# Kernel optimization log

Measured on AMD Instinct MI355X. Metric: run time of the kernel, lower is better.

Reference implementation:

```python
import jax, jax.numpy as jnp
import numpy as np

N_NODES = 100000
N_EDGES = 1600000
D_IN, D_HID, D_OUT = 128, 128, 128
EPS = 1e-12  # torch F.normalize eps


def _sage_conv(x, src, dst, Wl, bl, Wr):
    # PyG SAGEConv, aggr='mean', normalize=True:
    #   out = lin_l(mean_{j in N(i)} x_j) + lin_r(x_i); out = l2_normalize(out)
    msg = x[src]                                             # [E, D] gather
    agg = jax.ops.segment_sum(msg, dst, num_segments=N_NODES)
    cnt = jax.ops.segment_sum(jnp.ones((msg.shape[0],), x.dtype), dst,
                              num_segments=N_NODES)
    agg = agg / jnp.maximum(cnt, 1.0)[:, None]               # scatter-mean
    out = agg @ Wl + bl + x @ Wr
    norm = jnp.linalg.norm(out, axis=-1, keepdims=True)
    return out / jnp.maximum(norm, EPS)


def setup_inputs() -> dict:
    key = jax.random.key(0)
    ks = jax.random.split(key, 8)
    x = jax.random.normal(ks[0], (N_NODES, D_IN), dtype=jnp.float32)
    edge_index = jax.random.randint(ks[1], (2, N_EDGES), 0, N_NODES, dtype=jnp.int64)
    s1 = 1.0 / np.sqrt(D_IN)
    s2 = 1.0 / np.sqrt(D_HID)
    return {
        "x": x,
        "edge_index": edge_index,
        "W1l": jax.random.uniform(ks[2], (D_IN, D_HID), jnp.float32, -s1, s1),
        "b1": jnp.zeros((D_HID,), jnp.float32),
        "W1r": jax.random.uniform(ks[3], (D_IN, D_HID), jnp.float32, -s1, s1),
        "W2l": jax.random.uniform(ks[4], (D_HID, D_OUT), jnp.float32, -s2, s2),
        "b2": jnp.zeros((D_OUT,), jnp.float32),
        "W2r": jax.random.uniform(ks[5], (D_HID, D_OUT), jnp.float32, -s2, s2),
    }


def reference(x, edge_index, W1l, b1, W1r, W2l, b2, W2r):
    src, dst = edge_index[0], edge_index[1]
    h = _sage_conv(x, src, dst, W1l, b1, W1r)
    h = jax.nn.relu(h)
    # dropout is identity at inference (F.dropout with training=False)
    out = _sage_conv(h, src, dst, W2l, b2, W2r)
    return out
```

## Files before the change

### kernel.cpp

```cpp
#include <hip/hip_runtime.h>

static constexpr int D = 128;
static constexpr int CHUNK = 2048;
static constexpr int EB = 4096;
static constexpr int BSH = 8;

typedef __attribute__((ext_vector_type(8))) short short8;
typedef __attribute__((ext_vector_type(4))) float f32x4;

__device__ inline ushort f2bf(float f) {
  union { float f; uint u; } x; x.f = f;
  uint r = (x.u + 0x7fffu + ((x.u >> 16) & 1u)) >> 16;
  return (ushort)r;
}
__device__ inline float bfhi(uint u) {
  union { uint u; float f; } x; x.u = u & 0xffff0000u;
  return x.f;
}
__device__ inline float bflo(uint u) {
  union { uint u; float f; } x; x.u = u << 16;
  return x.f;
}


__global__ __launch_bounds__(256) void bucket_hist_kernel(
    const int* __restrict__ dsts, int E, int NB, int* __restrict__ bhist) {
  __shared__ int h[512];
  for (int i = threadIdx.x; i < NB; i += 256) h[i] = 0;
  __syncthreads();
  int base = blockIdx.x * EB;
  for (int t = threadIdx.x; t < EB; t += 256) {
    int e = base + t;
    if (e < E) atomicAdd(&h[dsts[e] >> BSH], 1);
  }
  __syncthreads();
  for (int i = threadIdx.x; i < NB; i += 256)
    if (h[i]) atomicAdd(&bhist[i], h[i]);
}

__global__ __launch_bounds__(512) void bucket_scan_kernel(
    const int* __restrict__ bhist, int NB, int* __restrict__ bstart,
    int* __restrict__ bcursor) {
  __shared__ int arr[512];
  int t = threadIdx.x;
  int v = (t < NB) ? bhist[t] : 0;
  arr[t] = v;
  __syncthreads();
  for (int off = 1; off < 512; off <<= 1) {
    int u = (t >= off) ? arr[t - off] : 0;
    __syncthreads();
    arr[t] += u;
    __syncthreads();
  }
  if (t < NB) {
    int s = arr[t] - v;
    bstart[t] = s;
    bcursor[t] = s;
  }
  if (t == NB - 1) bstart[NB] = arr[t];
}

__global__ __launch_bounds__(256) void bin_scatter_kernel(
    const int* __restrict__ srcs, const int* __restrict__ dsts, int E, int NB,
    int* __restrict__ bcursor, uint* __restrict__ bucket_arr) {
  __shared__ int h[512];
  __shared__ int gpos[512];
  __shared__ int run[512];
  for (int i = threadIdx.x; i < NB; i += 256) { h[i] = 0; run[i] = 0; }
  __syncthreads();
  int base = blockIdx.x * EB;
  for (int t = threadIdx.x; t < EB; t += 256) {
    int e = base + t;
    if (e < E) atomicAdd(&h[dsts[e] >> BSH], 1);
  }
  __syncthreads();
  for (int i = threadIdx.x; i < NB; i += 256)
    gpos[i] = h[i] ? atomicAdd(&bcursor[i], h[i]) : 0;
  __syncthreads();
  for (int t = threadIdx.x; t < EB; t += 256) {
    int e = base + t;
    if (e < E) {
      int dst = dsts[e];
      int src = srcs[e];
      int b = dst >> BSH;
      int r = atomicAdd(&run[b], 1);
      bucket_arr[gpos[b] + r] = (uint)src | ((uint)(dst & 255) << 17);
    }
  }
}

__global__ __launch_bounds__(256) void bucket_deg_kernel(
    const uint* __restrict__ bucket_arr, const int* __restrict__ bstart,
    int* __restrict__ deg, int N) {
  __shared__ int dcnt[256];
  int b = blockIdx.x;
  int n0 = b << BSH;
  int nn = min(256, N - n0);
  if (threadIdx.x < nn) dcnt[threadIdx.x] = 0;
  __syncthreads();
  int s = bstart[b], e = bstart[b + 1];
  for (int t = s + threadIdx.x; t < e; t += 256)
    atomicAdd(&dcnt[bucket_arr[t] >> 17], 1);
  __syncthreads();
  if (threadIdx.x < nn) deg[n0 + threadIdx.x] = dcnt[threadIdx.x];
}

__global__ __launch_bounds__(256) void csr_scatter_kernel(
    const uint* __restrict__ bucket_arr, const int* __restrict__ bstart,
    const int* __restrict__ row_start, int* __restrict__ csr_src, int N) {
  __shared__ int cur[256];
  int b = blockIdx.x;
  int n0 = b << BSH;
  int nn = min(256, N - n0);
  if (threadIdx.x < nn) cur[threadIdx.x] = row_start[n0 + threadIdx.x];
  __syncthreads();
  int s = bstart[b], e = bstart[b + 1];
  for (int t = s + threadIdx.x; t < e; t += 256) {
    uint p = bucket_arr[t];
    int pos = atomicAdd(&cur[p >> 17], 1);
    csr_src[pos] = (int)(p & 0x1FFFFu);
  }
}


__global__ __launch_bounds__(256) void scan_partial(const int* __restrict__ deg,
                                                    int* __restrict__ bsum, int N) {
  int base = blockIdx.x * CHUNK;
  int s = 0;
  for (int i = threadIdx.x; i < CHUNK; i += 256) {
    int g = base + i;
    if (g < N) s += deg[g];
  }
  __shared__ int red[256];
  red[threadIdx.x] = s;
  __syncthreads();
  for (int off = 128; off; off >>= 1) {
    if (threadIdx.x < off) red[threadIdx.x] += red[threadIdx.x + off];
    __syncthreads();
  }
  if (threadIdx.x == 0) bsum[blockIdx.x] = red[0];
}

__global__ __launch_bounds__(256) void scan_bsum(int* __restrict__ bsum, int G,
                                                 int* __restrict__ row_end) {
  __shared__ int arr[256];
  int t = threadIdx.x;
  int v = (t < G) ? bsum[t] : 0;
  arr[t] = v;
  __syncthreads();
  for (int off = 1; off < 256; off <<= 1) {
    int u = (t >= off) ? arr[t - off] : 0;
    __syncthreads();
    arr[t] += u;
    __syncthreads();
  }
  if (t < G) bsum[t] = arr[t] - v;
  if (t == 255) *row_end = arr[255];
}

__global__ __launch_bounds__(256) void scan_final(const int* __restrict__ deg,
                                                  const int* __restrict__ bsum,
                                                  int* __restrict__ row_start, int N) {
  int tid = threadIdx.x;
  int base = blockIdx.x * CHUNK + tid * 8;
  int d[8];
  int ts = 0;
#pragma unroll
  for (int j = 0; j < 8; ++j) {
    int g = base + j;
    int t = (g < N) ? deg[g] : 0;
    d[j] = ts;
    ts += t;
  }
  __shared__ int arr[256];
  arr[tid] = ts;
  __syncthreads();
  for (int off = 1; off < 256; off <<= 1) {
    int u = (tid >= off) ? arr[tid - off] : 0;
    __syncthreads();
    arr[tid] += u;
    __syncthreads();
  }
  int off0 = bsum[blockIdx.x] + arr[tid] - ts;
#pragma unroll
  for (int j = 0; j < 8; ++j) {
    int g = base + j;
    if (g < N) row_start[g] = off0 + d[j];
  }
}


__global__ __launch_bounds__(256) void cvt_bf16(const float* __restrict__ in,
                                                ushort* __restrict__ outb, int n8) {
  int i = blockIdx.x * blockDim.x + threadIdx.x;
  if (i >= n8) return;
  float4 a = *reinterpret_cast<const float4*>(in + (size_t)i * 8);
  float4 b = *reinterpret_cast<const float4*>(in + (size_t)i * 8 + 4);
  union { ushort s[8]; short8 v; } o;
  o.s[0] = f2bf(a.x); o.s[1] = f2bf(a.y); o.s[2] = f2bf(a.z); o.s[3] = f2bf(a.w);
  o.s[4] = f2bf(b.x); o.s[5] = f2bf(b.y); o.s[6] = f2bf(b.z); o.s[7] = f2bf(b.w);
  *reinterpret_cast<short8*>(outb + (size_t)i * 8) = o.v;
}

__global__ __launch_bounds__(256) void wprep(const float* __restrict__ W,
                                             ushort* __restrict__ WT) {
  int e = blockIdx.x * 256 + threadIdx.x;
  int k = e >> 7, n = e & 127;
  WT[n * 128 + k] = f2bf(W[e]);
}


#define ACC8(P, M)                                   \
  acc[0] += (M) * bflo(P.x); acc[1] += (M) * bfhi(P.x); \
  acc[2] += (M) * bflo(P.y); acc[3] += (M) * bfhi(P.y); \
  acc[4] += (M) * bflo(P.z); acc[5] += (M) * bfhi(P.z); \
  acc[6] += (M) * bflo(P.w); acc[7] += (M) * bfhi(P.w);

__global__ __launch_bounds__(256) void agg_kernel_bf16(
    const ushort* __restrict__ xb, const int* __restrict__ row_start,
    const int* __restrict__ csr_src, ushort* __restrict__ aggb, int N) {
  int wid = (blockIdx.x * blockDim.x + threadIdx.x) >> 6;
  int lane = threadIdx.x & 63;
  if (wid >= N) return;
  int r0 = row_start[wid];
  int r1 = row_start[wid + 1];
  const int grp = lane >> 4;
  const int sub = lane & 15;
  float acc[8];
#pragma unroll
  for (int k = 0; k < 8; ++k) acc[k] = 0.f;

  for (int base = r0; base < r1; base += 64) {
    int cnt = min(64, r1 - base);
    int idx = (lane < cnt) ? csr_src[base + lane] : 0;
    for (int j = 0; j < cnt; j += 16) {
      int s0 = __shfl(idx, j + grp);
      int s1 = __shfl(idx, j + 4 + grp);
      int s2 = __shfl(idx, j + 8 + grp);
      int s3 = __shfl(idx, j + 12 + grp);
      float m0 = (j + grp < cnt) ? 1.f : 0.f;
      float m1 = (j + 4 + grp < cnt) ? 1.f : 0.f;
      float m2 = (j + 8 + grp < cnt) ? 1.f : 0.f;
      float m3 = (j + 12 + grp < cnt) ? 1.f : 0.f;
      uint4 p0 = *reinterpret_cast<const uint4*>(xb + (size_t)s0 * D + sub * 8);
      uint4 p1 = *reinterpret_cast<const uint4*>(xb + (size_t)s1 * D + sub * 8);
      uint4 p2 = *reinterpret_cast<const uint4*>(xb + (size_t)s2 * D + sub * 8);
      uint4 p3 = *reinterpret_cast<const uint4*>(xb + (size_t)s3 * D + sub * 8);
      ACC8(p0, m0)
      ACC8(p1, m1)
      ACC8(p2, m2)
      ACC8(p3, m3)
    }
  }
#pragma unroll
  for (int k = 0; k < 8; ++k) {
    acc[k] += __shfl_xor(acc[k], 16);
    acc[k] += __shfl_xor(acc[k], 32);
  }
  float inv = 1.0f / (float)max(r1 - r0, 1);
  if (grp == 0) {
    union { ushort s[8]; short8 v; } o;
#pragma unroll
    for (int k = 0; k < 8; ++k) o.s[k] = f2bf(acc[k] * inv);
    *reinterpret_cast<short8*>(aggb + (size_t)wid * D + sub * 8) = o.v;
  }
}


__global__ __launch_bounds__(256) void sage_gemm_mfma(
    const ushort* __restrict__ Aagg, const ushort* __restrict__ Aself,
    const ushort* __restrict__ WTl, const ushort* __restrict__ WTr,
    const float* __restrict__ bias, float* __restrict__ outf,
    ushort* __restrict__ outb, int N, int relu) {
  __shared__ ushort A_lds[128 * 64];
  __shared__ ushort B_lds[128 * 64];
  const int tid = threadIdx.x;
  const int lane = tid & 63;
  const int wave = tid >> 6;
  const int block_row = blockIdx.x * 128;

  f32x4 acc[2][8];
#pragma unroll
  for (int i = 0; i < 2; ++i)
#pragma unroll
    for (int j = 0; j < 8; ++j) acc[i][j] = (f32x4){0.f, 0.f, 0.f, 0.f};

  for (int kc = 0; kc < 4; ++kc) {
    const ushort* Asrc = (kc < 2) ? Aagg : Aself;
    const ushort* Bsrc = (kc < 2) ? WTl : WTr;
    const int koff = (kc & 1) * 64;
    __syncthreads();
#pragma unroll
    for (int v = 0; v < 4; ++v) {
      int f = tid + v * 256;
      int row = f >> 3;
      int slot = f & 7;
      int sw = (slot ^ (row & 7)) * 8;
      int n = min(block_row + row, N - 1);
      *reinterpret_cast<short8*>(&A_lds[row * 64 + sw]) =
          *reinterpret_cast<const short8*>(Asrc + (size_t)n * D + koff + slot * 8);
      *reinterpret_cast<short8*>(&B_lds[row * 64 + sw]) =
          *reinterpret_cast<const short8*>(Bsrc + (size_t)row * D + koff + slot * 8);
    }
    __syncthreads();
#pragma unroll
    for (int s = 0; s < 2; ++s) {
      const int kb = lane >> 4;
      const int rsel = lane & 15;
      const int slot = s * 4 + kb;
      short8 a[2], b[8];
#pragma unroll
      for (int i = 0; i < 2; ++i) {
        int row = wave * 32 + i * 16 + rsel;
        a[i] = *reinterpret_cast<const short8*>(
            &A_lds[row * 64 + (slot ^ (row & 7)) * 8]);
      }
#pragma unroll
      for (int j = 0; j < 8; ++j) {
        int nr = j * 16 + rsel;
        b[j] = *reinterpret_cast<const short8*>(
            &B_lds[nr * 64 + (slot ^ (nr & 7)) * 8]);
      }
#pragma unroll
      for (int i = 0; i < 2; ++i)
#pragma unroll
        for (int j = 0; j < 8; ++j)
          acc[i][j] = __builtin_amdgcn_mfma_f32_16x16x32_bf16(a[i], b[j],
                                                              acc[i][j], 0, 0, 0);
    }
  }

  const int g = lane >> 4;
  const int cl = lane & 15;
  float bvals[8];
#pragma unroll
  for (int j = 0; j < 8; ++j) bvals[j] = bias[j * 16 + cl];
#pragma unroll
  for (int i = 0; i < 2; ++i) {
#pragma unroll
    for (int r = 0; r < 4; ++r) {
      float v[8];
      float ss = 0.f;
#pragma unroll
      for (int j = 0; j < 8; ++j) {
        v[j] = acc[i][j][r] + bvals[j];
        ss += v[j] * v[j];
      }
      ss += __shfl_xor(ss, 1);
      ss += __shfl_xor(ss, 2);
      ss += __shfl_xor(ss, 4);
      ss += __shfl_xor(ss, 8);
      float scale = 1.0f / fmaxf(sqrtf(ss), 1e-12f);
      int grow = block_row + wave * 32 + i * 16 + g * 4 + r;
      if (grow < N) {
        if (outb) {
#pragma unroll
          for (int j = 0; j < 8; ++j) {
            float o = v[j] * scale;
            if (relu) o = fmaxf(o, 0.f);
            outb[(size_t)grow * D + j * 16 + cl] = f2bf(o);
          }
        } else {
#pragma unroll
          for (int j = 0; j < 8; ++j)
            outf[(size_t)grow * D + j * 16 + cl] = v[j] * scale;
        }
      }
    }
  }
}


extern "C" void kernel_launch(void* const* d_in, const int* in_sizes, int n_in,
                              void* d_out, int out_size, void* d_ws, size_t ws_size,
                              hipStream_t stream) {
  const float* x = (const float*)d_in[0];
  const int* edges = (const int*)d_in[1];
  const float* W1l = (const float*)d_in[2];
  const float* b1 = (const float*)d_in[3];
  const float* W1r = (const float*)d_in[4];
  const float* W2l = (const float*)d_in[5];
  const float* b2 = (const float*)d_in[6];
  const float* W2r = (const float*)d_in[7];
  float* out = (float*)d_out;

  const int N = in_sizes[0] / D;
  const int E = in_sizes[1] / 2;
  const int G = (N + CHUNK - 1) / CHUNK;
  const int NB = (N + 255) >> BSH;
  const int GE = (E + EB - 1) / EB;

  const int* srcs = edges;
  const int* dsts = edges + E;

  char* ws = (char*)d_ws;
  ushort* xb   = (ushort*)ws;
  ushort* aggb = xb + (size_t)N * D;
  ushort* wt1l = aggb + (size_t)N * D;
  ushort* wt1r = wt1l + D * D;
  ushort* wt2l = wt1r + D * D;
  ushort* wt2r = wt2l + D * D;
  int* deg = (int*)(wt2r + D * D);
  int* row_start = deg + N;
  int* bsum = row_start + (N + 1);
  int* bhist = bsum + 256;
  int* bstart = bhist + 512;
  int* bcursor = bstart + 513;
  int* csr_src = bcursor + 512;
  uint* bucket_arr = (uint*)aggb;

  hipMemsetAsync(bhist, 0, 512 * sizeof(int), stream);
  bucket_hist_kernel<<<GE, 256, 0, stream>>>(dsts, E, NB, bhist);
  bucket_scan_kernel<<<1, 512, 0, stream>>>(bhist, NB, bstart, bcursor);
  bin_scatter_kernel<<<GE, 256, 0, stream>>>(srcs, dsts, E, NB, bcursor, bucket_arr);
  bucket_deg_kernel<<<NB, 256, 0, stream>>>(bucket_arr, bstart, deg, N);
  scan_partial<<<G, 256, 0, stream>>>(deg, bsum, N);
  scan_bsum<<<1, 256, 0, stream>>>(bsum, G, row_start + N);
  scan_final<<<G, 256, 0, stream>>>(deg, bsum, row_start, N);
  csr_scatter_kernel<<<NB, 256, 0, stream>>>(bucket_arr, bstart, row_start,
                                             csr_src, N);

  cvt_bf16<<<(N * D / 8 + 255) / 256, 256, 0, stream>>>(x, xb, N * D / 8);
  wprep<<<64, 256, 0, stream>>>(W1l, wt1l);
  wprep<<<64, 256, 0, stream>>>(W1r, wt1r);
  wprep<<<64, 256, 0, stream>>>(W2l, wt2l);
  wprep<<<64, 256, 0, stream>>>(W2r, wt2r);

  agg_kernel_bf16<<<(N + 3) / 4, 256, 0, stream>>>(xb, row_start, csr_src, aggb, N);
  sage_gemm_mfma<<<(N + 127) / 128, 256, 0, stream>>>(aggb, xb, wt1l, wt1r, b1,
                                                      nullptr, xb, N, 1);

  agg_kernel_bf16<<<(N + 3) / 4, 256, 0, stream>>>(xb, row_start, csr_src, aggb, N);
  sage_gemm_mfma<<<(N + 127) / 128, 256, 0, stream>>>(aggb, xb, wt2l, wt2r, b2,
                                                      out, nullptr, N, 0);
}
```

Measured before the change: 354.9 us.

## Fuse CSR build kernels, batch weight prep, use direct-to-LDS GEMM loads

Replaces the per-bucket degree count, three-pass global scan and CSR scatter with one per-bucket kernel. It counts degrees, does a local scan offset by the bucket start, and scatters sources, which cuts four kernel launches and the deg round trip. The four weight-prep launches become one. The aggregation switches to 32-bit byte offsets for gathers, and the GEMM tile loads use global_load_lds with the swizzle moved to the global address. The 32-bit offsets assume N*256 bytes fits in a uint, and the LDS-direct load needs correct waitcnt handling before the barrier.

```diff
diff --git a/kernel.cpp b/kernel.cpp
--- a/kernel.cpp
+++ b/kernel.cpp
@@ -1,7 +1,6 @@
 #include <hip/hip_runtime.h>
 
 static constexpr int D = 128;
-static constexpr int CHUNK = 2048;
 static constexpr int EB = 4096;
 static constexpr int BSH = 8;
 
@@ -21,6 +20,11 @@
   union { uint u; float f; } x; x.u = u << 16;
   return x.f;
 }
+
+#define GLOAD_LDS16(g, l)                                                  \
+  __builtin_amdgcn_global_load_lds(                                        \
+      (const __attribute__((address_space(1))) void*)(g),                  \
+      (__attribute__((address_space(3))) void*)(l), 16, 0, 0)
 
 
 __global__ __launch_bounds__(256) void bucket_hist_kernel(
@@ -89,103 +93,41 @@
   }
 }
 
-__global__ __launch_bounds__(256) void bucket_deg_kernel(
+__global__ __launch_bounds__(256) void csr_fused_kernel(
     const uint* __restrict__ bucket_arr, const int* __restrict__ bstart,
-    int* __restrict__ deg, int N) {
-  __shared__ int dcnt[256];
+    int* __restrict__ row_start, int* __restrict__ csr_src, int N, int NB) {
+  __shared__ int arr[256];
+  __shared__ int cur[256];
   int b = blockIdx.x;
+  int t = threadIdx.x;
   int n0 = b << BSH;
   int nn = min(256, N - n0);
-  if (threadIdx.x < nn) dcnt[threadIdx.x] = 0;
+  arr[t] = 0;
   __syncthreads();
   int s = bstart[b], e = bstart[b + 1];
-  for (int t = s + threadIdx.x; t < e; t += 256)
-    atomicAdd(&dcnt[bucket_arr[t] >> 17], 1);
-  __syncthreads();
-  if (threadIdx.x < nn) deg[n0 + threadIdx.x] = dcnt[threadIdx.x];
-}
-
-__global__ __launch_bounds__(256) void csr_scatter_kernel(
-    const uint* __restrict__ bucket_arr, const int* __restrict__ bstart,
-    const int* __restrict__ row_start, int* __restrict__ csr_src, int N) {
-  __shared__ int cur[256];
-  int b = blockIdx.x;
-  int n0 = b << BSH;
-  int nn = min(256, N - n0);
-  if (threadIdx.x < nn) cur[threadIdx.x] = row_start[n0 + threadIdx.x];
-  __syncthreads();
-  int s = bstart[b], e = bstart[b + 1];
-  for (int t = s + threadIdx.x; t < e; t += 256) {
-    uint p = bucket_arr[t];
+  for (int i = s + t; i < e; i += 256)
+    atomicAdd(&arr[bucket_arr[i] >> 17], 1);
+  __syncthreads();
+  int v = arr[t];
+  __syncthreads();
+  int run = v;
+  arr[t] = run;
+  __syncthreads();
+  for (int off = 1; off < 256; off <<= 1) {
+    int u = (t >= off) ? arr[t - off] : 0;
+    __syncthreads();
+    arr[t] += u;
+    __syncthreads();
+  }
+  int rs = bstart[b] + arr[t] - v;
+  cur[t] = rs;
+  if (t < nn) row_start[n0 + t] = rs;
+  if (b == NB - 1 && t == 0) row_start[N] = bstart[NB];
+  __syncthreads();
+  for (int i = s + t; i < e; i += 256) {
+    uint p = bucket_arr[i];
     int pos = atomicAdd(&cur[p >> 17], 1);
     csr_src[pos] = (int)(p & 0x1FFFFu);
-  }
-}
-
-
-__global__ __launch_bounds__(256) void scan_partial(const int* __restrict__ deg,
-                                                    int* __restrict__ bsum, int N) {
-  int base = blockIdx.x * CHUNK;
-  int s = 0;
-  for (int i = threadIdx.x; i < CHUNK; i += 256) {
-    int g = base + i;
-    if (g < N) s += deg[g];
-  }
-  __shared__ int red[256];
-  red[threadIdx.x] = s;
-  __syncthreads();
-  for (int off = 128; off; off >>= 1) {
-    if (threadIdx.x < off) red[threadIdx.x] += red[threadIdx.x + off];
-    __syncthreads();
-  }
-  if (threadIdx.x == 0) bsum[blockIdx.x] = red[0];
-}
-
-__global__ __launch_bounds__(256) void scan_bsum(int* __restrict__ bsum, int G,
-                                                 int* __restrict__ row_end) {
-  __shared__ int arr[256];
-  int t = threadIdx.x;
-  int v = (t < G) ? bsum[t] : 0;
-  arr[t] = v;
-  __syncthreads();
-  for (int off = 1; off < 256; off <<= 1) {
-    int u = (t >= off) ? arr[t - off] : 0;
-    __syncthreads();
-    arr[t] += u;
-    __syncthreads();
-  }
-  if (t < G) bsum[t] = arr[t] - v;
-  if (t == 255) *row_end = arr[255];
-}
-
-__global__ __launch_bounds__(256) void scan_final(const int* __restrict__ deg,
-                                                  const int* __restrict__ bsum,
-                                                  int* __restrict__ row_start, int N) {
-  int tid = threadIdx.x;
-  int base = blockIdx.x * CHUNK + tid * 8;
-  int d[8];
-  int ts = 0;
-#pragma unroll
-  for (int j = 0; j < 8; ++j) {
-    int g = base + j;
-    int t = (g < N) ? deg[g] : 0;
-    d[j] = ts;
-    ts += t;
-  }
-  __shared__ int arr[256];
-  arr[tid] = ts;
-  __syncthreads();
-  for (int off = 1; off < 256; off <<= 1) {
-    int u = (tid >= off) ? arr[tid - off] : 0;
-    __syncthreads();
-    arr[tid] += u;
-    __syncthreads();
-  }
-  int off0 = bsum[blockIdx.x] + arr[tid] - ts;
-#pragma unroll
-  for (int j = 0; j < 8; ++j) {
-    int g = base + j;
-    if (g < N) row_start[g] = off0 + d[j];
   }
 }
 
@@ -202,15 +144,19 @@
   *reinterpret_cast<short8*>(outb + (size_t)i * 8) = o.v;
 }
 
-__global__ __launch_bounds__(256) void wprep(const float* __restrict__ W,
-                                             ushort* __restrict__ WT) {
-  int e = blockIdx.x * 256 + threadIdx.x;
+__global__ __launch_bounds__(256) void wprep_all(
+    const float* __restrict__ W1l, const float* __restrict__ W1r,
+    const float* __restrict__ W2l, const float* __restrict__ W2r,
+    ushort* __restrict__ wt) {
+  int w = blockIdx.x >> 6;
+  const float* W = (w == 0) ? W1l : (w == 1) ? W1r : (w == 2) ? W2l : W2r;
+  int e = (blockIdx.x & 63) * 256 + threadIdx.x;
   int k = e >> 7, n = e & 127;
-  WT[n * 128 + k] = f2bf(W[e]);
-}
-
-
-#define ACC8(P, M)                                   \
+  wt[w * D * D + n * 128 + k] = f2bf(W[e]);
+}
+
+
+#define ACC8(P, M)                                      \
   acc[0] += (M) * bflo(P.x); acc[1] += (M) * bfhi(P.x); \
   acc[2] += (M) * bflo(P.y); acc[3] += (M) * bfhi(P.y); \
   acc[4] += (M) * bflo(P.z); acc[5] += (M) * bfhi(P.z); \
@@ -226,6 +172,8 @@
   int r1 = row_start[wid + 1];
   const int grp = lane >> 4;
   const int sub = lane & 15;
+  const uint loff = (uint)(sub << 4);
+  const char* xc = (const char*)xb;
   float acc[8];
 #pragma unroll
   for (int k = 0; k < 8; ++k) acc[k] = 0.f;
@@ -234,18 +182,18 @@
     int cnt = min(64, r1 - base);
     int idx = (lane < cnt) ? csr_src[base + lane] : 0;
     for (int j = 0; j < cnt; j += 16) {
-      int s0 = __shfl(idx, j + grp);
-      int s1 = __shfl(idx, j + 4 + grp);
-      int s2 = __shfl(idx, j + 8 + grp);
-      int s3 = __shfl(idx, j + 12 + grp);
+      uint o0 = ((uint)__shfl(idx, j + grp) << 8) + loff;
+      uint o1 = ((uint)__shfl(idx, j + 4 + grp) << 8) + loff;
+      uint o2 = ((uint)__shfl(idx, j + 8 + grp) << 8) + loff;
+      uint o3 = ((uint)__shfl(idx, j + 12 + grp) << 8) + loff;
       float m0 = (j + grp < cnt) ? 1.f : 0.f;
       float m1 = (j + 4 + grp < cnt) ? 1.f : 0.f;
       float m2 = (j + 8 + grp < cnt) ? 1.f : 0.f;
       float m3 = (j + 12 + grp < cnt) ? 1.f : 0.f;
-      uint4 p0 = *reinterpret_cast<const uint4*>(xb + (size_t)s0 * D + sub * 8);
-      uint4 p1 = *reinterpret_cast<const uint4*>(xb + (size_t)s1 * D + sub * 8);
-      uint4 p2 = *reinterpret_cast<const uint4*>(xb + (size_t)s2 * D + sub * 8);
-      uint4 p3 = *reinterpret_cast<const uint4*>(xb + (size_t)s3 * D + sub * 8);
+      uint4 p0 = *reinterpret_cast<const uint4*>(xc + o0);
+      uint4 p1 = *reinterpret_cast<const uint4*>(xc + o1);
+      uint4 p2 = *reinterpret_cast<const uint4*>(xc + o2);
+      uint4 p3 = *reinterpret_cast<const uint4*>(xc + o3);
       ACC8(p0, m0)
       ACC8(p1, m1)
       ACC8(p2, m2)
@@ -295,12 +243,12 @@
       int f = tid + v * 256;
       int row = f >> 3;
       int slot = f & 7;
-      int sw = (slot ^ (row & 7)) * 8;
+      int gs = slot ^ (row & 7);
       int n = min(block_row + row, N - 1);
-      *reinterpret_cast<short8*>(&A_lds[row * 64 + sw]) =
-          *reinterpret_cast<const short8*>(Asrc + (size_t)n * D + koff + slot * 8);
-      *reinterpret_cast<short8*>(&B_lds[row * 64 + sw]) =
-          *reinterpret_cast<const short8*>(Bsrc + (size_t)row * D + koff + slot * 8);
+      GLOAD_LDS16(Asrc + (size_t)n * D + koff + gs * 8,
+                  &A_lds[row * 64 + slot * 8]);
+      GLOAD_LDS16(Bsrc + (size_t)row * D + koff + gs * 8,
+                  &B_lds[row * 64 + slot * 8]);
     }
     __syncthreads();
 #pragma unroll
@@ -386,7 +334,6 @@
 
   const int N = in_sizes[0] / D;
   const int E = in_sizes[1] / 2;
-  const int G = (N + CHUNK - 1) / CHUNK;
   const int NB = (N + 255) >> BSH;
   const int GE = (E + EB - 1) / EB;
 
@@ -396,14 +343,9 @@
   char* ws = (char*)d_ws;
   ushort* xb   = (ushort*)ws;
   ushort* aggb = xb + (size_t)N * D;
-  ushort* wt1l = aggb + (size_t)N * D;
-  ushort* wt1r = wt1l + D * D;
-  ushort* wt2l = wt1r + D * D;
-  ushort* wt2r = wt2l + D * D;
-  int* deg = (int*)(wt2r + D * D);
-  int* row_start = deg + N;
-  int* bsum = row_start + (N + 1);
-  int* bhist = bsum + 256;
+  ushort* wt   = aggb + (size_t)N * D;
+  int* row_start = (int*)(wt + 4 * D * D);
+  int* bhist = row_start + (N + 1);
   int* bstart = bhist + 512;
   int* bcursor = bstart + 513;
   int* csr_src = bcursor + 512;
@@ -413,18 +355,16 @@
   bucket_hist_kernel<<<GE, 256, 0, stream>>>(dsts, E, NB, bhist);
   bucket_scan_kernel<<<1, 512, 0, stream>>>(bhist, NB, bstart, bcursor);
   bin_scatter_kernel<<<GE, 256, 0, stream>>>(srcs, dsts, E, NB, bcursor, bucket_arr);
-  bucket_deg_kernel<<<NB, 256, 0, stream>>>(bucket_arr, bstart, deg, N);
-  scan_partial<<<G, 256, 0, stream>>>(deg, bsum, N);
-  scan_bsum<<<1, 256, 0, stream>>>(bsum, G, row_start + N);
-  scan_final<<<G, 256, 0, stream>>>(deg, bsum, row_start, N);
-  csr_scatter_kernel<<<NB, 256, 0, stream>>>(bucket_arr, bstart, row_start,
-                                             csr_src, N);
+  csr_fused_kernel<<<NB, 256, 0, stream>>>(bucket_arr, bstart, row_start,
+                                           csr_src, N, NB);
 
   cvt_bf16<<<(N * D / 8 + 255) / 256, 256, 0, stream>>>(x, xb, N * D / 8);
-  wprep<<<64, 256, 0, stream>>>(W1l, wt1l);
-  wprep<<<64, 256, 0, stream>>>(W1r, wt1r);
-  wprep<<<64, 256, 0, stream>>>(W2l, wt2l);
-  wprep<<<64, 256, 0, stream>>>(W2r, wt2r);
+  wprep_all<<<256, 256, 0, stream>>>(W1l, W1r, W2l, W2r, wt);
+
+  ushort* wt1l = wt;
+  ushort* wt1r = wt + D * D;
+  ushort* wt2l = wt + 2 * D * D;
+  ushort* wt2r = wt + 3 * D * D;
 
   agg_kernel_bf16<<<(N + 3) / 4, 256, 0, stream>>>(xb, row_start, csr_src, aggb, N);
   sage_gemm_mfma<<<(N + 127) / 128, 256, 0, stream>>>(aggb, xb, wt1l, wt1r, b1,
```

Result: faster. 328.7 us (-7.4%).
